# Optimization experiments

Measured on AMD Instinct MI355X. Metric: run time of the kernel, lower is better.

The kernel has to match this reference:

```python
import jax, jax.numpy as jnp
import numpy as np
import math

B, N, C = 8, 4096, 768
H = 12
DH = C // H
M = 256
LN_EPS = 1e-5


def setup_inputs() -> dict:
    key = jax.random.key(0)
    ks = jax.random.split(key, 7)
    x = jax.random.normal(ks[0], (B, N, C), dtype=jnp.float32)
    # torch Linear weight [out,in]; store transposed for y = x @ W
    W_qkv = jax.random.normal(ks[1], (C, 3 * C), dtype=jnp.float32) * (1.0 / math.sqrt(C))
    W_proj = jax.random.normal(ks[2], (C, C), dtype=jnp.float32) * (1.0 / math.sqrt(C))
    b_proj = jnp.zeros((C,), dtype=jnp.float32)
    gamma = jnp.ones((C,), dtype=jnp.float32)
    beta = jnp.zeros((C,), dtype=jnp.float32)
    random_features = jax.random.normal(ks[3], (M, DH), dtype=jnp.float32) / math.sqrt(DH)
    return {"x": x, "W_qkv": W_qkv, "W_proj": W_proj, "b_proj": b_proj,
            "gamma": gamma, "beta": beta, "random_features": random_features}


def _phi(t, random_features):
    # t: [B, H, N, DH] -> [B, H, N, M]; phi(x) = exp(w·x - ||x||^2/2) / sqrt(M)
    norm_sq = 0.5 * jnp.sum(t * t, axis=-1, keepdims=True)
    proj = jnp.einsum('bhnd,md->bhnm', t, random_features)
    return jnp.exp(proj - norm_sq) * (1.0 / math.sqrt(M))


def reference(x, W_qkv, W_proj, b_proj, gamma, beta, random_features):
    b, n, c = x.shape
    qkv = (x @ W_qkv).reshape(b, n, 3, H, DH)
    qkv = jnp.transpose(qkv, (2, 0, 3, 1, 4))  # [3, B, H, N, DH]
    q, k, v = qkv[0], qkv[1], qkv[2]

    q_p = _phi(q, random_features)  # [B,H,N,M]
    k_p = _phi(k, random_features)  # [B,H,N,M]

    kv = jnp.einsum('bhnm,bhnd->bhmd', k_p, v)       # [B,H,M,DH]
    out = jnp.einsum('bhnm,bhmd->bhnd', q_p, kv)     # [B,H,N,DH]

    k_sum = jnp.sum(k_p, axis=2)                      # [B,H,M]
    normalizer = jnp.einsum('bhnm,bhm->bhn', q_p, k_sum)[..., None]
    out = out / (normalizer + 1e-6)

    x_attn = jnp.transpose(out, (0, 2, 1, 3)).reshape(b, n, c)
    x_attn = x_attn @ W_proj + b_proj
    # dropout is identity in eval / p=0

    y = x + x_attn
    mu = jnp.mean(y, axis=-1, keepdims=True)
    var = jnp.mean(jnp.square(y - mu), axis=-1, keepdims=True)
    return (y - mu) * jax.lax.rsqrt(var + LN_EPS) * gamma + beta
```

## Files before the change

### kernel.cpp

```cpp
#include <hip/hip_runtime.h>
#include <hip/hip_fp16.h>


#define LOG2E 1.44269504088896340736f

typedef _Float16 half8 __attribute__((ext_vector_type(8)));
typedef _Float16 half4_t __attribute__((ext_vector_type(4)));
typedef _Float16 half2_t __attribute__((ext_vector_type(2)));
typedef float f32x4 __attribute__((ext_vector_type(4)));

#if __has_builtin(__builtin_amdgcn_fdot2)
#define FDOT2(a, b, c) __builtin_amdgcn_fdot2((a), (b), (c), false)
#else
#define FDOT2(a, b, c) \
  ((float)(a)[0] * (float)(b)[0] + ((float)(a)[1] * (float)(b)[1] + (c)))
#endif

static __device__ __forceinline__ half2_t pk2(float a, float b) {
#if __has_builtin(__builtin_amdgcn_cvt_pkrtz)
  return __builtin_bit_cast(half2_t, __builtin_amdgcn_cvt_pkrtz(a, b));
#else
  half2_t r; r[0] = (_Float16)a; r[1] = (_Float16)b; return r;
#endif
}

__device__ __forceinline__ void glds16(const _Float16* g, _Float16* s) {
  __builtin_amdgcn_global_load_lds(
      (const __attribute__((address_space(1))) void*)g,
      (__attribute__((address_space(3))) unsigned int*)s,
      16, 0, 0);
}


__global__ __launch_bounds__(256)
void prep(const float* __restrict__ x, const float* __restrict__ Wqkv,
          const float* __restrict__ Wproj, const float* __restrict__ rfm,
          _Float16* __restrict__ x_h, _Float16* __restrict__ wqkvT,
          _Float16* __restrict__ wprojT, _Float16* __restrict__ rfh) {
  __shared__ _Float16 T[64][72];
  const int bid = blockIdx.x;
  if (bid < 12288) {
    long i = ((long)bid * 256 + threadIdx.x) * 8;
    float4 v0 = *(const float4*)(x + i);
    float4 v1 = *(const float4*)(x + i + 4);
    half8 h;
    h[0] = (_Float16)v0.x; h[1] = (_Float16)v0.y; h[2] = (_Float16)v0.z; h[3] = (_Float16)v0.w;
    h[4] = (_Float16)v1.x; h[5] = (_Float16)v1.y; h[6] = (_Float16)v1.z; h[7] = (_Float16)v1.w;
    *(half8*)(x_h + i) = h;
    return;
  }
  int tb = bid - 12288;
  if (tb < 576) {
    const float* src; _Float16* dst; int Csrc, r0, c0;
    if (tb < 432) {
      r0 = (tb / 36) * 64; c0 = (tb % 36) * 64; src = Wqkv; dst = wqkvT; Csrc = 2304;
    } else {
      int t2 = tb - 432;
      r0 = (t2 / 12) * 64; c0 = (t2 % 12) * 64; src = Wproj; dst = wprojT; Csrc = 768;
    }
    const int ri = threadIdx.x >> 4;
    const int ci = (threadIdx.x & 15) * 4;
#pragma unroll
    for (int rr = 0; rr < 4; ++rr) {
      float4 v = *(const float4*)(src + (long)(r0 + ri * 4 + rr) * Csrc + c0 + ci);
      T[ci + 0][ri * 4 + rr] = (_Float16)v.x;
      T[ci + 1][ri * 4 + rr] = (_Float16)v.y;
      T[ci + 2][ri * 4 + rr] = (_Float16)v.z;
      T[ci + 3][ri * 4 + rr] = (_Float16)v.w;
    }
    __syncthreads();
    const int wi = threadIdx.x >> 3;
    const int wj = (threadIdx.x & 7) * 8;
#pragma unroll
    for (int ww = 0; ww < 2; ++ww) {
      const int row = wi * 2 + ww;
      half8 h = *(const half8*)(&T[row][wj]);
      *(half8*)(dst + (long)(c0 + row) * 768 + r0 + wj) = h;
    }
  } else {
    int idx = (tb - 576) * 256 + threadIdx.x;
    if (idx < 16384) rfh[idx] = (_Float16)rfm[idx];
  }
}


__device__ __forceinline__ void stage_unit(const _Float16* __restrict__ G, int grow0,
                                           int kcol, _Float16* lds, int w, int l) {
#pragma unroll
  for (int j = 0; j < 2; ++j) {
    const int ci = w + j * 8;
    const int row = ci * 8 + (l >> 3);
    const int col8 = (l & 7) ^ (row & 7);
    glds16(G + (long)(grow0 + row) * 768 + kcol + col8 * 8, lds + ci * 512);
  }
}

static __device__ __forceinline__ half8 ldsw(const _Float16* buf, int r, int sl) {
  return *(const half8*)(buf + r * 64 + ((sl ^ (r & 7)) << 3));
}

__global__ __launch_bounds__(512)
void gemm_qkv(const _Float16* __restrict__ W, const _Float16* __restrict__ X,
              _Float16* __restrict__ qh, _Float16* __restrict__ kh,
              _Float16* __restrict__ vT,
              float* __restrict__ nsqLq, float* __restrict__ nsqLk) {
  __shared__ __align__(16) _Float16 SMEM[65536];
  _Float16* As = SMEM;
  _Float16* Bs = SMEM + 32768;
  const int tid = threadIdx.x;
  const int w = tid >> 6, l = tid & 63;
  const int lr = l & 15, kg = l >> 4;
  const int wr = w >> 2, wc = w & 3;

  const int bid = blockIdx.x;
  const int wg = (bid & 7) * 144 + (bid >> 3);
  const int m0 = (wg % 9) * 256;
  const int n0 = (wg / 9) * 256;

  stage_unit(W, m0,       0,  As,         w, l);
  stage_unit(X, n0,       0,  Bs,         w, l);
  stage_unit(X, n0 + 128, 0,  Bs + 8192,  w, l);
  stage_unit(W, m0 + 128, 0,  As + 8192,  w, l);
  stage_unit(W, m0,       64, As + 16384, w, l);
  stage_unit(X, n0,       64, Bs + 16384, w, l);
  stage_unit(X, n0 + 128, 64, Bs + 24576, w, l);
  asm volatile("s_waitcnt vmcnt(6)" ::: "memory");
  __builtin_amdgcn_s_barrier();

  f32x4 acc[8][4];
#pragma unroll
  for (int t = 0; t < 8; ++t)
#pragma unroll
    for (int u = 0; u < 4; ++u) acc[t][u] = (f32x4){0.f, 0.f, 0.f, 0.f};

  for (int kt = 0; kt < 12; ++kt) {
    const int c = kt & 1, o = c ^ 1;
    const _Float16* Ac = As + c * 16384;
    const _Float16* Bc = Bs + c * 16384;
    half8 aR[4][2], bR0[2][2], bR1[2][2];

#pragma unroll
    for (int i = 0; i < 4; ++i) {
      const int r = wr * 16 + i * 32 + lr;
      aR[i][0] = ldsw(Ac, r, kg);
      aR[i][1] = ldsw(Ac, r, 4 + kg);
    }
#pragma unroll
    for (int j = 0; j < 2; ++j) {
      const int r = wc * 16 + j * 64 + lr;
      bR0[j][0] = ldsw(Bc, r, kg);
      bR0[j][1] = ldsw(Bc, r, 4 + kg);
    }
    if (kt + 1 < 12)
      stage_unit(W, m0 + 128, (kt + 1) * 64, As + o * 16384 + 8192, w, l);
    __builtin_amdgcn_s_barrier();
    __builtin_amdgcn_s_setprio(1);
#pragma unroll
    for (int ks = 0; ks < 2; ++ks)
#pragma unroll
      for (int i = 0; i < 4; ++i)
#pragma unroll
        for (int j = 0; j < 2; ++j)
          acc[i][j] = __builtin_amdgcn_mfma_f32_16x16x32_f16(aR[i][ks], bR0[j][ks],
                                                             acc[i][j], 0, 0, 0);
    __builtin_amdgcn_s_setprio(0);
    __builtin_amdgcn_s_barrier();

#pragma unroll
    for (int j = 0; j < 2; ++j) {
      const int r = 128 + wc * 16 + j * 64 + lr;
      bR1[j][0] = ldsw(Bc, r, kg);
      bR1[j][1] = ldsw(Bc, r, 4 + kg);
    }
    if (kt + 2 < 12)
      stage_unit(W, m0, (kt + 2) * 64, As + c * 16384, w, l);
    __builtin_amdgcn_s_barrier();
    __builtin_amdgcn_s_setprio(1);
#pragma unroll
    for (int ks = 0; ks < 2; ++ks)
#pragma unroll
      for (int i = 0; i < 4; ++i)
#pragma unroll
        for (int j = 0; j < 2; ++j)
          acc[i][2 + j] = __builtin_amdgcn_mfma_f32_16x16x32_f16(aR[i][ks], bR1[j][ks],
                                                                 acc[i][2 + j], 0, 0, 0);
    __builtin_amdgcn_s_setprio(0);
    __builtin_amdgcn_s_barrier();

#pragma unroll
    for (int i = 0; i < 4; ++i) {
      const int r = 128 + wr * 16 + i * 32 + lr;
      aR[i][0] = ldsw(Ac, r, kg);
      aR[i][1] = ldsw(Ac, r, 4 + kg);
    }
    if (kt + 2 < 12)
      stage_unit(X, n0, (kt + 2) * 64, Bs + c * 16384, w, l);
    __builtin_amdgcn_s_barrier();
    __builtin_amdgcn_s_setprio(1);
#pragma unroll
    for (int ks = 0; ks < 2; ++ks)
#pragma unroll
      for (int i = 0; i < 4; ++i)
#pragma unroll
        for (int j = 0; j < 2; ++j)
          acc[4 + i][2 + j] = __builtin_amdgcn_mfma_f32_16x16x32_f16(aR[i][ks], bR1[j][ks],
                                                                     acc[4 + i][2 + j], 0, 0, 0);
    __builtin_amdgcn_s_setprio(0);
    __builtin_amdgcn_s_barrier();

    if (kt + 2 < 12)
      stage_unit(X, n0 + 128, (kt + 2) * 64, Bs + c * 16384 + 8192, w, l);
    if (kt < 10)
      asm volatile("s_waitcnt vmcnt(6)" ::: "memory");
    else
      asm volatile("s_waitcnt vmcnt(0)" ::: "memory");
    __builtin_amdgcn_s_barrier();
    __builtin_amdgcn_s_setprio(1);
#pragma unroll
    for (int ks = 0; ks < 2; ++ks)
#pragma unroll
      for (int i = 0; i < 4; ++i)
#pragma unroll
        for (int j = 0; j < 2; ++j)
          acc[4 + i][j] = __builtin_amdgcn_mfma_f32_16x16x32_f16(aR[i][ks], bR0[j][ks],
                                                                 acc[4 + i][j], 0, 0, 0);
    __builtin_amdgcn_s_setprio(0);
    __builtin_amdgcn_s_barrier();
  }

  const int which = (m0 >= 1536) ? 2 : ((m0 >= 768) ? 1 : 0);
  const int hbase = (m0 - which * 768) >> 6;
  const int b_ = n0 >> 12;
  const int nb = n0 & 4095;

  if (which < 2) {
    _Float16* dst = which ? kh : qh;
    float* nd = which ? nsqLk : nsqLq;
#pragma unroll
    for (int t = 0; t < 8; ++t) {
      const int m_ = wr * 16 + t * 32 + kg * 4;
#pragma unroll
      for (int u = 0; u < 4; ++u) {
        const int n_ = wc * 16 + u * 64 + lr;
        half2_t h01 = pk2(acc[t][u][0], acc[t][u][1]);
        half2_t h23 = pk2(acc[t][u][2], acc[t][u][3]);
        half4_t p4; p4[0] = h01[0]; p4[1] = h01[1]; p4[2] = h23[0]; p4[3] = h23[1];
        *(half4_t*)((char*)SMEM + n_ * 512 + (((m_ >> 3) ^ (n_ & 7)) << 4) +
                    (m_ & 4) * 2) = p4;
      }
    }
    __syncthreads();
    const int h2 = w >> 1;
    const int jj = l & 7;
    const long bhout = (long)(b_ * 12 + hbase + h2);
#pragma unroll
    for (int i = 0; i < 16; ++i) {
      const int n_ = (w & 1) * 128 + i * 8 + (l >> 3);
      const int phys = (h2 * 8 + jj) ^ (n_ & 7);
      half8 v = *(const half8*)((const char*)SMEM + n_ * 512 + phys * 16);
      *(half8*)(dst + (bhout * 4096 + nb + n_) * 64 + jj * 8) = v;
      float s = 0.f;
#pragma unroll
      for (int e = 0; e < 8; ++e) { float f = (float)v[e]; s += f * f; }
      s += __shfl_xor(s, 1);
      s += __shfl_xor(s, 2);
      s += __shfl_xor(s, 4);
      if (jj == 0) nd[bhout * 4096 + nb + n_] = 0.5f * s * LOG2E + 4.0f;
    }
  } else {
#pragma unroll
    for (int t = 0; t < 8; ++t) {
#pragma unroll
      for (int u = 0; u < 4; ++u) {
        const int n_ = wc * 16 + u * 64 + lr;
#pragma unroll
        for (int r = 0; r < 4; ++r) {
          const int m_ = wr * 16 + t * 32 + kg * 4 + r;
          *(_Float16*)((char*)SMEM + m_ * 512 + ((((n_ >> 3)) ^ (m_ & 7)) << 4) +
                       (n_ & 7) * 2) = (_Float16)acc[t][u][r];
        }
      }
    }
    __syncthreads();
#pragma unroll
    for (int i = 0; i < 16; ++i) {
      const int m_ = w * 32 + i * 2 + (l >> 5);
      const int c = l & 31;
      half8 v = *(const half8*)((const char*)SMEM + m_ * 512 + ((c ^ (m_ & 7)) << 4));
      const int h2 = m_ >> 6, d = m_ & 63;
      *(half8*)(vT + ((long)(b_ * 12 + hbase + h2) * 64 + d) * 4096 + nb + c * 8) = v;
    }
  }
}


__global__ __launch_bounds__(512)
void proj_ln(const _Float16* __restrict__ A, const _Float16* __restrict__ BT,
             const float* __restrict__ bias, const float* __restrict__ xres,
             const float* __restrict__ gamma, const float* __restrict__ beta,
             float* __restrict__ y) {
  __shared__ __align__(16) _Float16 Asm[64 * 768];
  __shared__ __align__(16) float lnS[64][8];
  __shared__ __align__(16) float lnQ[64][8];
  const int tid = threadIdx.x;
  const int w = tid >> 6, l = tid & 63;
  const int lr = l & 15, kg = l >> 4;
  const int m0 = blockIdx.x * 64;
  const int ncol0 = w * 96;

#pragma unroll
  for (int i = 0; i < 12; ++i) {
    const int sg = i * 512 + tid;
    const int row = sg / 96;
    const int p = sg - row * 96;
    glds16(A + (long)(m0 + row) * 768 + ((p ^ (row & 7)) << 3), Asm + sg * 8);
  }
  asm volatile("s_waitcnt vmcnt(0)" ::: "memory");
  __builtin_amdgcn_s_barrier();

  f32x4 acc[4][6];
#pragma unroll
  for (int mf = 0; mf < 4; ++mf)
#pragma unroll
    for (int nf = 0; nf < 6; ++nf) acc[mf][nf] = (f32x4){0.f, 0.f, 0.f, 0.f};

#pragma unroll 2
  for (int kc = 0; kc < 12; ++kc) {
    half8 bf[6][2];
#pragma unroll
    for (int nf = 0; nf < 6; ++nf)
#pragma unroll
      for (int ks = 0; ks < 2; ++ks)
        bf[nf][ks] = *(const half8*)(BT + (long)(ncol0 + nf * 16 + lr) * 768 +
                                     kc * 64 + ks * 32 + kg * 8);
    half8 af[4][2];
#pragma unroll
    for (int mf = 0; mf < 4; ++mf) {
      const int r = mf * 16 + lr;
#pragma unroll
      for (int ks = 0; ks < 2; ++ks)
        af[mf][ks] = *(const half8*)(Asm + r * 768 +
                                     (((kc * 8 + ks * 4 + kg) ^ (lr & 7)) << 3));
    }
#pragma unroll
    for (int ks = 0; ks < 2; ++ks)
#pragma unroll
      for (int mf = 0; mf < 4; ++mf)
#pragma unroll
        for (int nf = 0; nf < 6; ++nf)
          acc[mf][nf] = __builtin_amdgcn_mfma_f32_16x16x32_f16(af[mf][ks], bf[nf][ks],
                                                               acc[mf][nf], 0, 0, 0);
  }

  float bv[6], gv[6], betv[6];
#pragma unroll
  for (int nf = 0; nf < 6; ++nf) {
    const int col = ncol0 + nf * 16 + lr;
    bv[nf] = bias[col]; gv[nf] = gamma[col]; betv[nf] = beta[col];
  }
#pragma unroll
  for (int mf = 0; mf < 4; ++mf)
#pragma unroll
    for (int r = 0; r < 4; ++r) {
      const int row = mf * 16 + kg * 4 + r;
#pragma unroll
      for (int nf = 0; nf < 6; ++nf)
        acc[mf][nf][r] += bv[nf] + xres[(long)(m0 + row) * 768 + ncol0 + nf * 16 + lr];
    }
#pragma unroll
  for (int mf = 0; mf < 4; ++mf)
#pragma unroll
    for (int r = 0; r < 4; ++r) {
      float s = 0.f, q = 0.f;
#pragma unroll
      for (int nf = 0; nf < 6; ++nf) {
        const float v = acc[mf][nf][r];
        s += v; q += v * v;
      }
      s += __shfl_xor(s, 1); q += __shfl_xor(q, 1);
      s += __shfl_xor(s, 2); q += __shfl_xor(q, 2);
      s += __shfl_xor(s, 4); q += __shfl_xor(q, 4);
      s += __shfl_xor(s, 8); q += __shfl_xor(q, 8);
      if (lr == 0) {
        const int row = mf * 16 + kg * 4 + r;
        lnS[row][w] = s; lnQ[row][w] = q;
      }
    }
  __syncthreads();
#pragma unroll
  for (int mf = 0; mf < 4; ++mf)
#pragma unroll
    for (int r = 0; r < 4; ++r) {
      const int row = mf * 16 + kg * 4 + r;
      f32x4 s0 = *(const f32x4*)&lnS[row][0];
      f32x4 s1 = *(const f32x4*)&lnS[row][4];
      f32x4 q0 = *(const f32x4*)&lnQ[row][0];
      f32x4 q1 = *(const f32x4*)&lnQ[row][4];
      const float s = s0[0] + s0[1] + s0[2] + s0[3] + s1[0] + s1[1] + s1[2] + s1[3];
      const float q = q0[0] + q0[1] + q0[2] + q0[3] + q1[0] + q1[1] + q1[2] + q1[3];
      const float mu = s * (1.f / 768.f);
      const float var = q * (1.f / 768.f) - mu * mu;
      const float rstd = rsqrtf(var + 1e-5f);
#pragma unroll
      for (int nf = 0; nf < 6; ++nf)
        y[(long)(m0 + row) * 768 + ncol0 + nf * 16 + lr] =
            (acc[mf][nf][r] - mu) * rstd * gv[nf] + betv[nf];
    }
}


__global__ __launch_bounds__(256)
void kv_fused(const _Float16* __restrict__ kh, const _Float16* __restrict__ vT,
              const _Float16* __restrict__ rfh, const float* __restrict__ nsqLk,
              _Float16* __restrict__ kvpart, float* __restrict__ kspart) {
  __shared__ __align__(16) _Float16 P[256 * 72];
  const int chunk = blockIdx.x, bh = blockIdx.y;
  const int tid = threadIdx.x, w = tid >> 6, l = tid & 63;
  const int lr = l & 15, kg = l >> 4;
  const long khbase = (long)bh * 4096 * 64;
  const long vtbase = (long)bh * 64 * 4096;
  const half2_t ONES = {(_Float16)1.f, (_Float16)1.f};

  half8 rf[4][2];
#pragma unroll
  for (int u = 0; u < 4; ++u)
#pragma unroll
    for (int ks = 0; ks < 2; ++ks)
      rf[u][ks] = *(const half8*)(rfh + (w * 64 + u * 16 + lr) * 64 + ks * 32 + kg * 8);

  f32x4 kvacc[4][4];
#pragma unroll
  for (int mt = 0; mt < 4; ++mt)
#pragma unroll
    for (int dt = 0; dt < 4; ++dt) kvacc[mt][dt] = (f32x4){0.f, 0.f, 0.f, 0.f};
  float ksacc[4] = {0.f, 0.f, 0.f, 0.f};

  for (int t8 = 0; t8 < 8; ++t8) {
    const int nt = chunk * 512 + t8 * 64;

    half8 af[4][2];
#pragma unroll
    for (int tt = 0; tt < 4; ++tt)
#pragma unroll
      for (int ks = 0; ks < 2; ++ks)
        af[tt][ks] = *(const half8*)(kh + khbase + (long)(nt + tt * 16 + lr) * 64 +
                                     ks * 32 + kg * 8);

    f32x4 sacc[4][4];
#pragma unroll
    for (int tt = 0; tt < 4; ++tt)
#pragma unroll
      for (int u = 0; u < 4; ++u) sacc[tt][u] = (f32x4){0.f, 0.f, 0.f, 0.f};
#pragma unroll
    for (int ks = 0; ks < 2; ++ks)
#pragma unroll
      for (int tt = 0; tt < 4; ++tt)
#pragma unroll
        for (int u = 0; u < 4; ++u)
          sacc[tt][u] = __builtin_amdgcn_mfma_f32_16x16x32_f16(af[tt][ks], rf[u][ks],
                                                               sacc[tt][u], 0, 0, 0);
    float4 nsq4[4];
#pragma unroll
    for (int tt = 0; tt < 4; ++tt)
      nsq4[tt] = *(const float4*)(nsqLk + (long)bh * 4096 + nt + tt * 16 + kg * 4);
#pragma unroll
    for (int tt = 0; tt < 4; ++tt)
#pragma unroll
      for (int u = 0; u < 4; ++u) {
        float e0 = exp2f(sacc[tt][u][0] * LOG2E - nsq4[tt].x);
        float e1 = exp2f(sacc[tt][u][1] * LOG2E - nsq4[tt].y);
        float e2 = exp2f(sacc[tt][u][2] * LOG2E - nsq4[tt].z);
        float e3 = exp2f(sacc[tt][u][3] * LOG2E - nsq4[tt].w);
        half2_t h01 = pk2(e0, e1), h23 = pk2(e2, e3);
        half4_t p4; p4[0] = h01[0]; p4[1] = h01[1]; p4[2] = h23[0]; p4[3] = h23[1];
        *(half4_t*)(P + (w * 64 + u * 16 + lr) * 72 + tt * 16 + kg * 4) = p4;
      }

#pragma unroll
    for (int ks = 0; ks < 2; ++ks) {
      half8 pa[4], bv[4];
#pragma unroll
      for (int mt = 0; mt < 4; ++mt)
        pa[mt] = *(const half8*)(P + (w * 64 + mt * 16 + lr) * 72 + ks * 32 + kg * 8);
#pragma unroll
      for (int dt = 0; dt < 4; ++dt)
        bv[dt] = *(const half8*)(vT + vtbase + (long)(dt * 16 + lr) * 4096 + nt +
                                 ks * 32 + kg * 8);
#pragma unroll
      for (int mt = 0; mt < 4; ++mt)
#pragma unroll
        for (int dt = 0; dt < 4; ++dt)
          kvacc[mt][dt] = __builtin_amdgcn_mfma_f32_16x16x32_f16(pa[mt], bv[dt],
                                                                 kvacc[mt][dt], 0, 0, 0);
#pragma unroll
      for (int mt = 0; mt < 4; ++mt) {
        const half2_t* pp = (const half2_t*)&pa[mt];
#pragma unroll
        for (int p = 0; p < 4; ++p) ksacc[mt] = FDOT2(pp[p], ONES, ksacc[mt]);
      }
    }
  }

#pragma unroll
  for (int mt = 0; mt < 4; ++mt) {
    float v = ksacc[mt];
    v += __shfl_xor(v, 16);
    v += __shfl_xor(v, 32);
    if (l < 16) kspart[((bh * 8 + chunk) << 8) + w * 64 + mt * 16 + l] = v;
  }
#pragma unroll
  for (int mt = 0; mt < 4; ++mt)
#pragma unroll
    for (int dt = 0; dt < 4; ++dt)
#pragma unroll
      for (int r = 0; r < 4; ++r)
        kvpart[(((long)(bh * 8 + chunk) * 256) + w * 64 + mt * 16 + kg * 4 + r) * 64 +
               dt * 16 + lr] = (_Float16)kvacc[mt][dt][r];
}


__global__ __launch_bounds__(256)
void reduce_all(const _Float16* __restrict__ kvpart, const float* __restrict__ kspart,
                _Float16* __restrict__ kvT, _Float16* __restrict__ ksumh) {
  if (blockIdx.x < 6144) {
    long i = (long)blockIdx.x * 256 + threadIdx.x;
    const int bh = (int)(i >> 14);
    const int rem = (int)(i & 16383);
    const int m = rem >> 6, d = rem & 63;
    float s = 0.f;
#pragma unroll
    for (int c = 0; c < 8; ++c)
      s += (float)kvpart[(((long)bh * 8 + c) * 256 + m) * 64 + d];
    kvT[(long)bh * 16384 + d * 256 + m] = (_Float16)s;
  } else {
    int i = (blockIdx.x - 6144) * 256 + threadIdx.x;
    int bh = i >> 8, m = i & 255;
    float s = 0.f;
#pragma unroll
    for (int c = 0; c < 8; ++c) s += kspart[((bh * 8 + c) << 8) + m];
    ksumh[i] = (_Float16)s;
  }
}


__global__ __launch_bounds__(256)
void attn_fused(const _Float16* __restrict__ qh, const _Float16* __restrict__ rfh,
                const float* __restrict__ nsqLq, const _Float16* __restrict__ kvT,
                const _Float16* __restrict__ ksumh, _Float16* __restrict__ attn) {
  __shared__ __align__(16) _Float16 KV[64 * 264];
  __shared__ __align__(16) _Float16 KS[256];
  __shared__ __align__(16) _Float16 P[64 * 264];
  __shared__ __align__(16) float NS[64];
  const int chunk = blockIdx.x, bh = blockIdx.y;
  const int b = bh / 12, h = bh % 12;
  const int tid = threadIdx.x, w = tid >> 6, l = tid & 63;
  const int lr = l & 15, kg = l >> 4;

  {
    const int d = tid >> 2, mb = (tid & 3) * 64;
#pragma unroll
    for (int j = 0; j < 8; ++j)
      *(half8*)(KV + d * 264 + mb + j * 8) =
          *(const half8*)(kvT + (long)bh * 16384 + d * 256 + mb + j * 8);
    if (tid < 32) *(half8*)(KS + tid * 8) = *(const half8*)(ksumh + bh * 256 + tid * 8);
  }

  half8 rf[4][2];
#pragma unroll
  for (int mt = 0; mt < 4; ++mt)
#pragma unroll
    for (int ks = 0; ks < 2; ++ks)
      rf[mt][ks] = *(const half8*)(rfh + (w * 64 + mt * 16 + lr) * 64 + ks * 32 + kg * 8);

  for (int t8 = 0; t8 < 4; ++t8) {
    const int nt = chunk * 256 + t8 * 64;
    __syncthreads();

    half8 bq[4][2];
#pragma unroll
    for (int tt = 0; tt < 4; ++tt)
#pragma unroll
      for (int ks = 0; ks < 2; ++ks)
        bq[tt][ks] = *(const half8*)(qh + ((long)bh * 4096 + nt + tt * 16 + lr) * 64 +
                                     ks * 32 + kg * 8);

    f32x4 sacc[4][4];
#pragma unroll
    for (int mt = 0; mt < 4; ++mt)
#pragma unroll
      for (int tt = 0; tt < 4; ++tt) sacc[mt][tt] = (f32x4){0.f, 0.f, 0.f, 0.f};
#pragma unroll
    for (int ks = 0; ks < 2; ++ks)
#pragma unroll
      for (int mt = 0; mt < 4; ++mt)
#pragma unroll
        for (int tt = 0; tt < 4; ++tt)
          sacc[mt][tt] = __builtin_amdgcn_mfma_f32_16x16x32_f16(rf[mt][ks], bq[tt][ks],
                                                                sacc[mt][tt], 0, 0, 0);
    float nsqv[4];
#pragma unroll
    for (int tt = 0; tt < 4; ++tt)
      nsqv[tt] = nsqLq[(long)bh * 4096 + nt + tt * 16 + lr];
#pragma unroll
    for (int mt = 0; mt < 4; ++mt)
#pragma unroll
      for (int tt = 0; tt < 4; ++tt) {
        float e0 = exp2f(sacc[mt][tt][0] * LOG2E - nsqv[tt]);
        float e1 = exp2f(sacc[mt][tt][1] * LOG2E - nsqv[tt]);
        float e2 = exp2f(sacc[mt][tt][2] * LOG2E - nsqv[tt]);
        float e3 = exp2f(sacc[mt][tt][3] * LOG2E - nsqv[tt]);
        half2_t h01 = pk2(e0, e1), h23 = pk2(e2, e3);
        half4_t p4; p4[0] = h01[0]; p4[1] = h01[1]; p4[2] = h23[0]; p4[3] = h23[1];
        *(half4_t*)(P + (tt * 16 + lr) * 264 + w * 64 + mt * 16 + kg * 4) = p4;
      }
    __syncthreads();

    f32x4 oacc[4];
#pragma unroll
    for (int u = 0; u < 4; ++u) oacc[u] = (f32x4){0.f, 0.f, 0.f, 0.f};
    float nacc = 0.f;
#pragma unroll
    for (int ks = 0; ks < 8; ++ks) {
      half8 ap = *(const half8*)(P + (w * 16 + lr) * 264 + ks * 32 + kg * 8);
      half8 kv8 = *(const half8*)(KS + ks * 32 + kg * 8);
      const half2_t* a2 = (const half2_t*)&ap;
      const half2_t* k2 = (const half2_t*)&kv8;
#pragma unroll
      for (int p = 0; p < 4; ++p) nacc = FDOT2(a2[p], k2[p], nacc);
#pragma unroll
      for (int u = 0; u < 4; ++u) {
        half8 bkv = *(const half8*)(KV + (u * 16 + lr) * 264 + ks * 32 + kg * 8);
        oacc[u] = __builtin_amdgcn_mfma_f32_16x16x32_f16(ap, bkv, oacc[u], 0, 0, 0);
      }
    }
    nacc += __shfl_xor(nacc, 16);
    nacc += __shfl_xor(nacc, 32);
    if (l < 16) NS[w * 16 + l] = nacc;
    f32x4 n4 = *(const f32x4*)(NS + w * 16 + kg * 4);
    float inv[4];
#pragma unroll
    for (int r = 0; r < 4; ++r) inv[r] = 1.f / (n4[r] + 1e-6f);
#pragma unroll
    for (int u = 0; u < 4; ++u)
#pragma unroll
      for (int r = 0; r < 4; ++r)
        attn[((long)b * 4096 + nt + w * 16 + kg * 4 + r) * 768 + h * 64 + u * 16 + lr] =
            (_Float16)(oacc[u][r] * inv[r]);
  }
}


extern "C" void kernel_launch(void* const* d_in, const int* in_sizes, int n_in,
                              void* d_out, int out_size, void* d_ws, size_t ws_size,
                              hipStream_t stream) {
  const float* x = (const float*)d_in[0];
  const float* Wqkv = (const float*)d_in[1];
  const float* Wproj = (const float*)d_in[2];
  const float* bproj = (const float*)d_in[3];
  const float* gamma = (const float*)d_in[4];
  const float* beta = (const float*)d_in[5];
  const float* rfm = (const float*)d_in[6];

  char* ws = (char*)d_ws;
  size_t off = 0;
  auto alloc = [&](size_t bytes) -> void* {
    void* p = ws + off;
    off += (bytes + 255) & ~(size_t)255;
    return p;
  };
  char* regionA = (char*)alloc(50331648ULL);
  _Float16* x_h = (_Float16*)regionA;
  _Float16* kvpart = (_Float16*)regionA;
  _Float16* attn = (_Float16*)regionA;

  _Float16* wqkvT = (_Float16*)alloc(1769472ULL * 2);
  _Float16* wprojT = (_Float16*)alloc(589824ULL * 2);
  _Float16* rfh = (_Float16*)alloc(16384ULL * 2);
  _Float16* qh = (_Float16*)alloc(25165824ULL * 2);
  _Float16* kh = (_Float16*)alloc(25165824ULL * 2);
  _Float16* vT = (_Float16*)alloc(25165824ULL * 2);
  float* nsqLq = (float*)alloc(393216ULL * 4);
  float* nsqLk = (float*)alloc(393216ULL * 4);
  float* kspart = (float*)alloc(96ULL * 8 * 256 * 4);
  _Float16* kvT = (_Float16*)alloc(96ULL * 16384 * 2);
  _Float16* ksumh = (_Float16*)alloc(96ULL * 256 * 2);

  float* y = (float*)d_out;

  prep<<<12928, 256, 0, stream>>>(x, Wqkv, Wproj, rfm, x_h, wqkvT, wprojT, rfh);
  gemm_qkv<<<1152, 512, 0, stream>>>(wqkvT, x_h, qh, kh, vT, nsqLq, nsqLk);
  kv_fused<<<dim3(8, 96), 256, 0, stream>>>(kh, vT, rfh, nsqLk, kvpart, kspart);
  reduce_all<<<6240, 256, 0, stream>>>(kvpart, kspart, kvT, ksumh);
  attn_fused<<<dim3(16, 96), 256, 0, stream>>>(qh, rfh, nsqLq, kvT, ksumh, attn);
  proj_ln<<<512, 512, 0, stream>>>(attn, wprojT, bproj, x, gamma, beta, y);
}
```

Baseline: 561.5 us.

## Load all LDS fragments up front and cut QKV GEMM barriers per k-step

Restructures the QKV GEMM main loop. All A and B fragments (both 128-row halves) are now read from LDS at the start of each k-iteration, and the four MFMA quadrants run back to back instead of being split into four phases, each fenced by two barriers. The global-to-LDS staging for the next tiles is grouped after a single barrier, and the prologue staging order is changed so the second A half arrives early enough. This cuts barrier and synchronisation overhead and gives longer MFMA runs, at the cost of more live fragment registers, which could hurt occupancy, and less interleaving of LDS reads with MFMA.

Measured after the change: 578.1 us. 3.0% more time.

```diff
diff --git a/kernel.cpp b/kernel.cpp
--- a/kernel.cpp
+++ b/kernel.cpp
@@ -118,9 +118,9 @@
   const int n0 = (wg / 9) * 256;
 
   stage_unit(W, m0,       0,  As,         w, l);
+  stage_unit(W, m0 + 128, 0,  As + 8192,  w, l);
   stage_unit(X, n0,       0,  Bs,         w, l);
   stage_unit(X, n0 + 128, 0,  Bs + 8192,  w, l);
-  stage_unit(W, m0 + 128, 0,  As + 8192,  w, l);
   stage_unit(W, m0,       64, As + 16384, w, l);
   stage_unit(X, n0,       64, Bs + 16384, w, l);
   stage_unit(X, n0 + 128, 64, Bs + 24576, w, l);
@@ -137,94 +137,80 @@
     const int c = kt & 1, o = c ^ 1;
     const _Float16* Ac = As + c * 16384;
     const _Float16* Bc = Bs + c * 16384;
-    half8 aR[4][2], bR0[2][2], bR1[2][2];
+    half8 a0[4][2], a1[4][2], b0[2][2], b1[2][2];
 
 #pragma unroll
     for (int i = 0; i < 4; ++i) {
       const int r = wr * 16 + i * 32 + lr;
-      aR[i][0] = ldsw(Ac, r, kg);
-      aR[i][1] = ldsw(Ac, r, 4 + kg);
+      a0[i][0] = ldsw(Ac, r, kg);
+      a0[i][1] = ldsw(Ac, r, 4 + kg);
     }
 #pragma unroll
     for (int j = 0; j < 2; ++j) {
       const int r = wc * 16 + j * 64 + lr;
-      bR0[j][0] = ldsw(Bc, r, kg);
-      bR0[j][1] = ldsw(Bc, r, 4 + kg);
+      b0[j][0] = ldsw(Bc, r, kg);
+      b0[j][1] = ldsw(Bc, r, 4 + kg);
+    }
+#pragma unroll
+    for (int j = 0; j < 2; ++j) {
+      const int r = 128 + wc * 16 + j * 64 + lr;
+      b1[j][0] = ldsw(Bc, r, kg);
+      b1[j][1] = ldsw(Bc, r, 4 + kg);
+    }
+#pragma unroll
+    for (int i = 0; i < 4; ++i) {
+      const int r = 128 + wr * 16 + i * 32 + lr;
+      a1[i][0] = ldsw(Ac, r, kg);
+      a1[i][1] = ldsw(Ac, r, 4 + kg);
     }
     if (kt + 1 < 12)
       stage_unit(W, m0 + 128, (kt + 1) * 64, As + o * 16384 + 8192, w, l);
+
+    __builtin_amdgcn_s_setprio(1);
+#pragma unroll
+    for (int ks = 0; ks < 2; ++ks)
+#pragma unroll
+      for (int i = 0; i < 4; ++i)
+#pragma unroll
+        for (int j = 0; j < 2; ++j)
+          acc[i][j] = __builtin_amdgcn_mfma_f32_16x16x32_f16(a0[i][ks], b0[j][ks],
+                                                             acc[i][j], 0, 0, 0);
+#pragma unroll
+    for (int ks = 0; ks < 2; ++ks)
+#pragma unroll
+      for (int i = 0; i < 4; ++i)
+#pragma unroll
+        for (int j = 0; j < 2; ++j)
+          acc[i][2 + j] = __builtin_amdgcn_mfma_f32_16x16x32_f16(a0[i][ks], b1[j][ks],
+                                                                 acc[i][2 + j], 0, 0, 0);
+#pragma unroll
+    for (int ks = 0; ks < 2; ++ks)
+#pragma unroll
+      for (int i = 0; i < 4; ++i)
+#pragma unroll
+        for (int j = 0; j < 2; ++j)
+          acc[4 + i][2 + j] = __builtin_amdgcn_mfma_f32_16x16x32_f16(a1[i][ks], b1[j][ks],
+                                                                     acc[4 + i][2 + j], 0, 0, 0);
+#pragma unroll
+    for (int ks = 0; ks < 2; ++ks)
+#pragma unroll
+      for (int i = 0; i < 4; ++i)
+#pragma unroll
+        for (int j = 0; j < 2; ++j)
+          acc[4 + i][j] = __builtin_amdgcn_mfma_f32_16x16x32_f16(a1[i][ks], b0[j][ks],
+                                                                 acc[4 + i][j], 0, 0, 0);
+    __builtin_amdgcn_s_setprio(0);
+
     __builtin_amdgcn_s_barrier();
-    __builtin_amdgcn_s_setprio(1);
-#pragma unroll
-    for (int ks = 0; ks < 2; ++ks)
-#pragma unroll
-      for (int i = 0; i < 4; ++i)
-#pragma unroll
-        for (int j = 0; j < 2; ++j)
-          acc[i][j] = __builtin_amdgcn_mfma_f32_16x16x32_f16(aR[i][ks], bR0[j][ks],
-                                                             acc[i][j], 0, 0, 0);
-    __builtin_amdgcn_s_setprio(0);
-    __builtin_amdgcn_s_barrier();
-
-#pragma unroll
-    for (int j = 0; j < 2; ++j) {
-      const int r = 128 + wc * 16 + j * 64 + lr;
-      bR1[j][0] = ldsw(Bc, r, kg);
-      bR1[j][1] = ldsw(Bc, r, 4 + kg);
-    }
-    if (kt + 2 < 12)
+    if (kt + 2 < 12) {
       stage_unit(W, m0, (kt + 2) * 64, As + c * 16384, w, l);
-    __builtin_amdgcn_s_barrier();
-    __builtin_amdgcn_s_setprio(1);
-#pragma unroll
-    for (int ks = 0; ks < 2; ++ks)
-#pragma unroll
-      for (int i = 0; i < 4; ++i)
-#pragma unroll
-        for (int j = 0; j < 2; ++j)
-          acc[i][2 + j] = __builtin_amdgcn_mfma_f32_16x16x32_f16(aR[i][ks], bR1[j][ks],
-                                                                 acc[i][2 + j], 0, 0, 0);
-    __builtin_amdgcn_s_setprio(0);
-    __builtin_amdgcn_s_barrier();
-
-#pragma unroll
-    for (int i = 0; i < 4; ++i) {
-      const int r = 128 + wr * 16 + i * 32 + lr;
-      aR[i][0] = ldsw(Ac, r, kg);
-      aR[i][1] = ldsw(Ac, r, 4 + kg);
-    }
-    if (kt + 2 < 12)
       stage_unit(X, n0, (kt + 2) * 64, Bs + c * 16384, w, l);
-    __builtin_amdgcn_s_barrier();
-    __builtin_amdgcn_s_setprio(1);
-#pragma unroll
-    for (int ks = 0; ks < 2; ++ks)
-#pragma unroll
-      for (int i = 0; i < 4; ++i)
-#pragma unroll
-        for (int j = 0; j < 2; ++j)
-          acc[4 + i][2 + j] = __builtin_amdgcn_mfma_f32_16x16x32_f16(aR[i][ks], bR1[j][ks],
-                                                                     acc[4 + i][2 + j], 0, 0, 0);
-    __builtin_amdgcn_s_setprio(0);
-    __builtin_amdgcn_s_barrier();
-
-    if (kt + 2 < 12)
       stage_unit(X, n0 + 128, (kt + 2) * 64, Bs + c * 16384 + 8192, w, l);
+    }
     if (kt < 10)
       asm volatile("s_waitcnt vmcnt(6)" ::: "memory");
     else
       asm volatile("s_waitcnt vmcnt(0)" ::: "memory");
-    __builtin_amdgcn_s_barrier();
-    __builtin_amdgcn_s_setprio(1);
-#pragma unroll
-    for (int ks = 0; ks < 2; ++ks)
-#pragma unroll
-      for (int i = 0; i < 4; ++i)
-#pragma unroll
-        for (int j = 0; j < 2; ++j)
-          acc[4 + i][j] = __builtin_amdgcn_mfma_f32_16x16x32_f16(aR[i][ks], bR0[j][ks],
-                                                                 acc[4 + i][j], 0, 0, 0);
-    __builtin_amdgcn_s_setprio(0);
     __builtin_amdgcn_s_barrier();
   }
 
```
